# Optimization experiments

Measured on AMD Instinct MI355X. Metric: run time of the kernel, lower is better.

Reference implementation:

```python
import jax, jax.numpy as jnp
import numpy as np

RANGE_DISP = 32
IND_INPUT_VIEW = np.array([1, 9]) - 1  # 0-based indices of the two input views
TOTAL_VIEWS = 9                         # an_sparse + an_novel
FEAT_CH = 64


def conv2d(x, w, b):
    # x: (N, Cin, H, W), w: (Cout, Cin, kh, kw), SAME padding, stride 1
    y = jax.lax.conv_general_dilated(x, w, (1, 1), 'SAME',
                                     dimension_numbers=('NCHW', 'OIHW', 'NCHW'))
    return y + b[None, :, None, None]


def unfold_1xK(x, K):
    # torch.nn.functional.unfold(x, kernel_size=(1, K)) for x: (M, C, H, W)
    # -> (M, C, K, H*(W-K+1)), column index = h*(W-K+1) + w (row-major).
    M, C, H, W = x.shape
    out_w = W - K + 1
    cols = jnp.arange(out_w)[None, :] + jnp.arange(K)[:, None]  # (K, out_w)
    y = x[:, :, :, cols]             # (M, C, H, K, out_w)
    y = y.transpose(0, 1, 3, 2, 4)   # (M, C, K, H, out_w)
    return y.reshape(M, C, K, H * out_w)


def setup_inputs() -> dict:
    key = jax.random.key(0)
    ks = jax.random.split(key, 24)
    b, an_sparse, an_novel, rp = 2, 2, 7, 32
    K = RANGE_DISP
    ps = rp + K - 1  # 63

    def rn(k, shape, s=1.0):
        return jax.random.normal(k, shape, dtype=jnp.float32) * s

    W = 0.05  # weight init scale
    return {
        'lf_sparse':        rn(ks[0], (b, an_sparse, rp, ps)),
        'flow_sparse':      rn(ks[1], (b, an_sparse, rp, ps)),
        'warped_lf_sparse': rn(ks[2], (b, an_sparse, rp, ps)),
        'patch_left':       rn(ks[3], (b, an_novel, rp, rp)),
        'patch_right':      rn(ks[4], (b, an_novel, rp, rp)),
        # FlowRefNet: 3 -> 64 -> 64 -> 64, 3x3 convs, SAME
        'fr_w1': rn(ks[5], (FEAT_CH, 3, 3, 3), W), 'fr_b1': jnp.zeros((FEAT_CH,), jnp.float32),
        'fr_w2': rn(ks[6], (FEAT_CH, FEAT_CH, 3, 3), W), 'fr_b2': jnp.zeros((FEAT_CH,), jnp.float32),
        'fr_w3': rn(ks[7], (FEAT_CH, FEAT_CH, 3, 3), W), 'fr_b3': jnp.zeros((FEAT_CH,), jnp.float32),
        # MlpNet: per-disparity MLP 67 -> 64 -> 64 -> 1 (weight head) + conf head 64 -> 1
        'mlp_w1': rn(ks[8], (67, 64), W), 'mlp_b1': jnp.zeros((64,), jnp.float32),
        'mlp_w2': rn(ks[9], (64, 64), W), 'mlp_b2': jnp.zeros((64,), jnp.float32),
        'mlp_w3': rn(ks[10], (64, 1), W), 'mlp_b3': jnp.zeros((1,), jnp.float32),
        'conf_w': rn(ks[11], (64, 1), W), 'conf_b': jnp.zeros((1,), jnp.float32),
        # ViewRefNet: 3 -> 64 -> 64 -> 1 convs, residual on novel patch
        'vr_w1': rn(ks[12], (FEAT_CH, 3, 3, 3), W), 'vr_b1': jnp.zeros((FEAT_CH,), jnp.float32),
        'vr_w2': rn(ks[13], (FEAT_CH, FEAT_CH, 3, 3), W), 'vr_b2': jnp.zeros((FEAT_CH,), jnp.float32),
        'vr_w3': rn(ks[14], (1, FEAT_CH, 3, 3), W), 'vr_b3': jnp.zeros((1,), jnp.float32),
    }


def reference(lf_sparse, flow_sparse, warped_lf_sparse, patch_left, patch_right,
              fr_w1, fr_b1, fr_w2, fr_b2, fr_w3, fr_b3,
              mlp_w1, mlp_b1, mlp_w2, mlp_b2, mlp_w3, mlp_b3, conf_w, conf_b,
              vr_w1, vr_b1, vr_w2, vr_b2, vr_w3, vr_b3):
    b, an_sparse, rp, ps = lf_sparse.shape
    an_novel = patch_left.shape[1]
    K = RANGE_DISP
    N = rp * rp

    lf = lf_sparse.reshape(b * an_sparse, 1, rp, ps)
    fl = flow_sparse.reshape(b * an_sparse, 1, rp, ps)
    wp = warped_lf_sparse.reshape(b * an_sparse, 1, rp, ps)

    # FlowRefNet: flow-feature extraction
    h = jax.nn.relu(conv2d(jnp.concatenate([fl, lf, wp], axis=1), fr_w1, fr_b1))
    h = jax.nn.relu(conv2d(h, fr_w2, fr_b2))
    feat = jax.nn.relu(conv2d(h, fr_w3, fr_b3))  # (b*as, 64, rp, ps)

    # angular code: input-view index minus novel-view index
    ind_novel = np.delete(np.arange(TOTAL_VIEWS), IND_INPUT_VIEW)
    ang = jnp.asarray(IND_INPUT_VIEW[None, :] - ind_novel[:, None], dtype=lf.dtype)  # (an, as)
    spatial = (jnp.arange(K) - K // 2).astype(lf.dtype)  # (K,)

    # EPI windows via unfold(kernel=(1, K))
    flow_unf = unfold_1xK(fl, K)[:, 0]  # (b*as, K, N)
    feat_unf = unfold_1xK(feat, K)      # (b*as, 64, K, N)

    sh = (b, an_novel, an_sparse)
    f_flow = jnp.broadcast_to(flow_unf.reshape(b, 1, an_sparse, 1, K, N),  sh + (1, K, N))
    f_feat = jnp.broadcast_to(feat_unf.reshape(b, 1, an_sparse, FEAT_CH, K, N), sh + (FEAT_CH, K, N))
    f_spat = jnp.broadcast_to(spatial.reshape(1, 1, 1, 1, K, 1),           sh + (1, K, N))
    f_ang  = jnp.broadcast_to(ang.reshape(1, an_novel, an_sparse, 1, 1, 1), sh + (1, K, N))
    features = jnp.concatenate([f_flow, f_feat, f_spat, f_ang], axis=3)  # (b, an, as, 67, K, N)
    # -> (b*an*as*N, K, 67) matching permute(0,3,2,1).reshape in torch
    features = features.transpose(0, 1, 2, 5, 4, 3).reshape(-1, K, 67)

    # MlpNet: per-disparity weight + per-sample confidence
    h1 = jax.nn.relu(features @ mlp_w1 + mlp_b1)
    h2 = jax.nn.relu(h1 @ mlp_w2 + mlp_b2)          # (M2, K, 64)
    weight = (h2 @ mlp_w3 + mlp_b3)[..., 0]         # (M2, K)
    conf = (h2.mean(axis=1) @ conf_w + conf_b)[..., 0]  # (M2,)

    weight = jax.nn.softmax(weight.reshape(b, an_novel, an_sparse, N, K), axis=-1)
    confs = jax.nn.softmax(conf.reshape(b, an_novel, an_sparse, N), axis=2)

    # disparity-weighted combination over EPI windows
    epi = unfold_1xK(lf, K)[:, 0].reshape(b, an_sparse, K, N)
    nv = jnp.einsum('bskn,bvsnk->bvsn', epi, weight)   # (b, an, as, N)
    novel = (nv * confs).sum(axis=2)                   # (b, an, N)

    # ViewRefNet: residual refinement
    pn = novel.reshape(b * an_novel, 1, rp, rp)
    pl = patch_left.reshape(b * an_novel, 1, rp, rp)
    pr = patch_right.reshape(b * an_novel, 1, rp, rp)
    g = jax.nn.relu(conv2d(jnp.concatenate([pn, pl, pr], axis=1), vr_w1, vr_b1))
    g = jax.nn.relu(conv2d(g, vr_w2, vr_b2))
    res = conv2d(g, vr_w3, vr_b3)
    out = pn + res
    return out.reshape(b, an_novel, rp, rp)
```

## Files before the change

kernel.cpp:

```cpp
#include <hip/hip_runtime.h>

typedef unsigned short u16;
typedef unsigned int u32;
typedef __bf16 bf16x8 __attribute__((ext_vector_type(8)));
typedef float f32x4 __attribute__((ext_vector_type(4)));
typedef u16 u16x8 __attribute__((ext_vector_type(8)));

__device__ __forceinline__ u16 f2bf(float f) {
    __bf16 h = (__bf16)f;
    return __builtin_bit_cast(u16, h);
}
__device__ __forceinline__ float bf2f(u16 u) {
    unsigned int x = ((unsigned int)u) << 16;
    return __builtin_bit_cast(float, x);
}

union FragU { u16x8 u; bf16x8 v; };

constexpr size_t WB2F  = 0;
constexpr size_t WB3F  = 18432;
constexpr size_t WBV2  = 36864;
constexpr size_t W1T   = 55296;
constexpr size_t W2T   = 57344;
constexpr size_t X1    = 59392;
constexpr size_t X2    = 317440;
constexpr size_t FEATBF= 575488;
constexpr size_t NVOFF = 833536;
constexpr size_t CFOFF = 862208;
constexpr size_t NOVEL = 890880;
constexpr size_t Y1    = 905216;
constexpr size_t Y2    = 1363968;

__global__ __launch_bounds__(256) void conv1feat_kernel(
    const float* __restrict__ in0, const float* __restrict__ in1,
    const float* __restrict__ in2,
    const float* __restrict__ wts, const float* __restrict__ bias,
    u16* __restrict__ out,
    const float* __restrict__ frw2, const float* __restrict__ frw3,
    const float* __restrict__ vrw2,
    const float* __restrict__ mw1, const float* __restrict__ mw2,
    u16* __restrict__ wb2, u16* __restrict__ wb3, u16* __restrict__ wbv,
    u16* __restrict__ w1t, u16* __restrict__ w2t)
{
    constexpr int W = 63, NPX = 2016, H = 32;
    const int t = threadIdx.x;
    if (blockIdx.z == 4) {
        const int tid = (blockIdx.y * 8 + blockIdx.x) * 256 + t;
        for (int i = tid; i < 36864; i += 16384) {
            int tap = i >> 12, och = (i >> 6) & 63, cin = i & 63;
            size_t s = (size_t)och * 576 + cin * 9 + tap;
            wb2[i] = f2bf(frw2[s]);
            wb3[i] = f2bf(frw3[s]);
            wbv[i] = f2bf(vrw2[s]);
        }
        for (int i = tid; i < 4096; i += 16384) {
            int col = i >> 6, r = i & 63;
            w1t[i] = f2bf(mw1[(1 + r) * 64 + col]);
            w2t[i] = f2bf(mw2[r * 64 + col]);
        }
        return;
    }
    const int px = blockIdx.y * 256 + t;
    const int m = blockIdx.z;
    const int og = blockIdx.x;
    if (px >= NPX) return;
    const int y = px / W, x = px - y * W;

    float acc[8];
#pragma unroll
    for (int oc = 0; oc < 8; ++oc) acc[oc] = bias[og * 8 + oc];

#pragma unroll
    for (int cin = 0; cin < 3; ++cin) {
        const float* ip = (cin == 0 ? in0 : (cin == 1 ? in1 : in2)) + (size_t)m * NPX;
        float tap[9];
#pragma unroll
        for (int dy = 0; dy < 3; ++dy) {
            int yy = y + dy - 1;
            bool ry = (yy >= 0) && (yy < H);
#pragma unroll
            for (int dx = 0; dx < 3; ++dx) {
                int xx = x + dx - 1;
                tap[dy * 3 + dx] = (ry && xx >= 0 && xx < W) ? ip[yy * W + xx] : 0.f;
            }
        }
#pragma unroll
        for (int oc = 0; oc < 8; ++oc) {
            const float* wr = wts + (size_t)(og * 8 + oc) * 27 + cin * 9;
#pragma unroll
            for (int j = 0; j < 9; ++j) acc[oc] = fmaf(tap[j], wr[j], acc[oc]);
        }
    }
    u16x8 pk;
#pragma unroll
    for (int oc = 0; oc < 8; ++oc) pk[oc] = f2bf(fmaxf(acc[oc], 0.f));
    *(u16x8*)(out + ((size_t)m * NPX + px) * 64 + og * 8) = pk;
}

template<int W, int NPX>
__global__ __launch_bounds__(256) void convmfma_kernel(
    const u16* __restrict__ in, const u16* __restrict__ wbf,
    const float* __restrict__ bias, u16* __restrict__ out)
{
    constexpr int H = 32;
    const int t = threadIdx.x;
    const int base = blockIdx.x * 64;
    const int m = blockIdx.y;
    const int w = t >> 6, lane = t & 63, q = lane >> 4, l15 = lane & 15;

    const u16* im = in + (size_t)m * NPX * 64;
    const int pxA = base + w * 16 + l15;
    const int yA = pxA / W, xA = pxA - yA * W;
    const bool pxok = (pxA < NPX);

    f32x4 acc[4];
#pragma unroll
    for (int nt = 0; nt < 4; ++nt) acc[nt] = f32x4{0.f, 0.f, 0.f, 0.f};

#pragma unroll
    for (int tap = 0; tap < 9; ++tap) {
        const int dy = tap / 3 - 1, dx = tap % 3 - 1;
        const bool valid = pxok && (yA + dy >= 0) && (yA + dy < H)
                                && (xA + dx >= 0) && (xA + dx < W);
        const u16* ap = im + (size_t)(pxA + dy * W + dx) * 64;
        FragU a0, a1;
        if (valid) {
            a0 = *(const FragU*)(ap + q * 8);
            a1 = *(const FragU*)(ap + 32 + q * 8);
        } else {
#pragma unroll
            for (int jj = 0; jj < 8; ++jj) { a0.u[jj] = 0; a1.u[jj] = 0; }
        }
#pragma unroll
        for (int nt = 0; nt < 4; ++nt) {
            const u16* bp = wbf + tap * 4096 + (nt * 16 + l15) * 64;
            FragU b0 = *(const FragU*)(bp + q * 8);
            FragU b1 = *(const FragU*)(bp + 32 + q * 8);
            acc[nt] = __builtin_amdgcn_mfma_f32_16x16x32_bf16(a0.v, b0.v, acc[nt], 0, 0, 0);
            acc[nt] = __builtin_amdgcn_mfma_f32_16x16x32_bf16(a1.v, b1.v, acc[nt], 0, 0, 0);
        }
    }

#pragma unroll
    for (int nt = 0; nt < 4; ++nt) {
        const float bb = bias[nt * 16 + l15];
#pragma unroll
        for (int e = 0; e < 4; ++e) {
            int pxs = base + w * 16 + q * 4 + e;
            if (pxs < NPX)
                out[((size_t)m * NPX + pxs) * 64 + nt * 16 + l15] =
                    f2bf(fmaxf(acc[nt][e] + bb, 0.f));
        }
    }
}

__global__ __launch_bounds__(256, 2) void mlp_mfma_kernel(
    const float* __restrict__ lf, const float* __restrict__ flow,
    const u16* __restrict__ feat,
    const u16* __restrict__ w1t, const u16* __restrict__ w2t,
    const float* __restrict__ w1, const float* __restrict__ b1,
    const float* __restrict__ b2,
    const float* __restrict__ w3, const float* __restrict__ b3g,
    const float* __restrict__ cw, const float* __restrict__ cbg,
    float* __restrict__ nv_out, float* __restrict__ cf_out)
{
    constexpr int SBS = 72;
    __shared__ __align__(16) float s_vec[7 * 64];
    __shared__ __align__(16) float s_flow[256];
    __shared__ __align__(16) float s_epi[256];
    __shared__ __align__(16) u16 s_base[256 * SBS];

    const int t = threadIdx.x;
    const int blk = blockIdx.x;
    const int v = blk >> 9;
    const int r9_ = blk & 511;
    const int bs = r9_ >> 7;
    const int n0 = (r9_ & 127) * 8;
    const int b = bs >> 1, s = bs & 1;
    const int w = t >> 6, lane = t & 63, q = lane >> 4, l15 = lane & 15;

    if (t < 64) {
        s_vec[t]       = b1[t];
        s_vec[64 + t]  = b2[t];
        s_vec[128 + t] = w3[t];
        s_vec[192 + t] = cw[t];
        s_vec[256 + t] = w1[t];
        s_vec[320 + t] = w1[65 * 64 + t];
        s_vec[384 + t] = w1[66 * 64 + t];
    }
    {
        int nl = t >> 5, k = t & 31;
        int n = n0 + nl;
        int a = (bs * 32 + (n >> 5)) * 63 + (n & 31) + k;
        s_flow[t] = flow[a];
        s_epi[t]  = lf[a];
    }
    __syncthreads();

    const float b3s = b3g[0];
    const float cbs = cbg[0];

    FragU w1b[2][4];
#pragma unroll
    for (int ks = 0; ks < 2; ++ks)
#pragma unroll
        for (int nt = 0; nt < 4; ++nt)
            w1b[ks][nt] = *(const FragU*)(w1t + (nt * 16 + l15) * 64 + ks * 32 + q * 8);

    float w1r0pl[4], w1r65pl[4], b1pl[4];
#pragma unroll
    for (int nt = 0; nt < 4; ++nt) {
        int j1 = nt * 16 + l15;
        w1r0pl[nt]  = s_vec[256 + j1];
        w1r65pl[nt] = s_vec[320 + j1];
        b1pl[nt]    = s_vec[j1];
    }

#pragma unroll
    for (int mt = 0; mt < 4; ++mt) {
        const int rbase = w * 64 + mt * 16;
        FragU af[2];
        {
            int r = rbase + l15;
            int n = n0 + (r >> 5);
            int pos = (n >> 5) * 63 + (n & 31) + (r & 31);
            const u16* fp = feat + ((size_t)bs * 2016 + pos) * 64;
            af[0] = *(const FragU*)(fp + q * 8);
            af[1] = *(const FragU*)(fp + 32 + q * 8);
        }
        f32x4 flow4 = *(const f32x4*)(s_flow + rbase + q * 4);
#pragma unroll
        for (int nt = 0; nt < 4; ++nt) {
            f32x4 d = {0.f, 0.f, 0.f, 0.f};
            d = __builtin_amdgcn_mfma_f32_16x16x32_bf16(af[0].v, w1b[0][nt].v, d, 0, 0, 0);
            d = __builtin_amdgcn_mfma_f32_16x16x32_bf16(af[1].v, w1b[1][nt].v, d, 0, 0, 0);
#pragma unroll
            for (int e = 0; e < 4; ++e) {
                int r = rbase + q * 4 + e;
                int k = r & 31;
                float val = d[e] + flow4[e] * w1r0pl[nt]
                          + (float)(k - 16) * w1r65pl[nt] + b1pl[nt];
                s_base[r * SBS + nt * 16 + l15] = f2bf(val);
            }
        }
    }
    __syncthreads();

    FragU w2a[4][2];
#pragma unroll
    for (int mt = 0; mt < 4; ++mt)
#pragma unroll
        for (int ks = 0; ks < 2; ++ks)
            w2a[mt][ks] = *(const FragU*)(w2t + (mt * 16 + l15) * 64 + ks * 32 + q * 8);

    float w66pl[2][8];
#pragma unroll
    for (int ks = 0; ks < 2; ++ks)
#pragma unroll
        for (int jj = 0; jj < 8; ++jj)
            w66pl[ks][jj] = s_vec[384 + ks * 32 + q * 8 + jj];

    float b2pl[4][4], w3pl[4][4], cwpl[4][4];
#pragma unroll
    for (int mt = 0; mt < 4; ++mt)
#pragma unroll
        for (int e = 0; e < 4; ++e) {
            b2pl[mt][e] = s_vec[64 + mt * 16 + q * 4 + e];
            w3pl[mt][e] = s_vec[128 + mt * 16 + q * 4 + e];
            cwpl[mt][e] = s_vec[192 + mt * 16 + q * 4 + e];
        }
    float epi_pl[4];
#pragma unroll
    for (int nt = 0; nt < 4; ++nt) epi_pl[nt] = s_epi[w * 64 + nt * 16 + l15];

    const float ang = (s == 0) ? -(float)(v + 1) : (float)(7 - v);
    f32x4 acc[4][4];
#pragma unroll
    for (int nt = 0; nt < 4; ++nt) {
        FragU bfr[2];
#pragma unroll
        for (int ks = 0; ks < 2; ++ks) {
            const u16x8 raw = *(const u16x8*)(s_base + (w * 64 + nt * 16 + l15) * SBS + ks * 32 + q * 8);
#pragma unroll
            for (int jj = 0; jj < 8; ++jj) {
                float xv = bf2f(raw[jj]);
                float hv = fmaxf(xv + ang * w66pl[ks][jj], 0.f);
                bfr[ks].u[jj] = f2bf(hv);
            }
        }
#pragma unroll
        for (int mt = 0; mt < 4; ++mt) {
            f32x4 d = {0.f, 0.f, 0.f, 0.f};
            d = __builtin_amdgcn_mfma_f32_16x16x32_bf16(w2a[mt][0].v, bfr[0].v, d, 0, 0, 0);
            d = __builtin_amdgcn_mfma_f32_16x16x32_bf16(w2a[mt][1].v, bfr[1].v, d, 0, 0, 0);
            acc[mt][nt] = d;
        }
    }
    float wl[4], cfl[4];
#pragma unroll
    for (int nt = 0; nt < 4; ++nt) {
        float wls = 0.f, cfs = 0.f;
#pragma unroll
        for (int mt = 0; mt < 4; ++mt)
#pragma unroll
            for (int e = 0; e < 4; ++e) {
                float h2 = fmaxf(acc[mt][nt][e] + b2pl[mt][e], 0.f);
                wls += h2 * w3pl[mt][e];
                cfs += h2 * cwpl[mt][e];
            }
        wls += __shfl_xor(wls, 16); wls += __shfl_xor(wls, 32);
        cfs += __shfl_xor(cfs, 16); cfs += __shfl_xor(cfs, 32);
        wl[nt]  = wls + b3s;
        cfl[nt] = cfs;
    }
#pragma unroll
    for (int ni = 0; ni < 2; ++ni) {
        float a0 = wl[ni * 2], a1 = wl[ni * 2 + 1];
        float mx = fmaxf(a0, a1);
#pragma unroll
        for (int msk = 1; msk <= 8; msk <<= 1) mx = fmaxf(mx, __shfl_xor(mx, msk));
        float e0 = __expf(a0 - mx), e1 = __expf(a1 - mx);
        float ssum = e0 + e1;
        float nvp = e0 * epi_pl[ni * 2] + e1 * epi_pl[ni * 2 + 1];
        float cfp = cfl[ni * 2] + cfl[ni * 2 + 1];
#pragma unroll
        for (int msk = 1; msk <= 8; msk <<= 1) {
            ssum += __shfl_xor(ssum, msk);
            nvp  += __shfl_xor(nvp, msk);
            cfp  += __shfl_xor(cfp, msk);
        }
        if (lane == 0) {
            int n = n0 + w * 2 + ni;
            size_t idx = ((size_t)(b * 7 + v) * 2 + s) * 1024 + n;
            nv_out[idx] = nvp / ssum;
            cf_out[idx] = cfp * (1.f / 32.f) + cbs;
        }
    }
}

__global__ __launch_bounds__(256) void refconv1_kernel(
    const float* __restrict__ nv, const float* __restrict__ cf,
    const float* __restrict__ pl, const float* __restrict__ pr,
    const float* __restrict__ wts, const float* __restrict__ bias,
    u16* __restrict__ out, float* __restrict__ novel)
{
    __shared__ float pn[10][32];
    const int t = threadIdx.x;
    const int og = blockIdx.x, pt = blockIdx.y, m = blockIdx.z;
    const int y0 = pt * 8;

    for (int i = t; i < 320; i += 256) {
        int ri = i >> 5, col = i & 31;
        int gy = y0 - 1 + ri;
        float vv = 0.f;
        if (gy >= 0 && gy < 32) {
            int n = gy * 32 + col;
            size_t i0 = ((size_t)m * 2) * 1024 + n;
            size_t i1 = i0 + 1024;
            float c0 = cf[i0], c1 = cf[i1];
            float mx = fmaxf(c0, c1);
            float e0 = __expf(c0 - mx), e1 = __expf(c1 - mx);
            vv = (e0 * nv[i0] + e1 * nv[i1]) / (e0 + e1);
        }
        pn[ri][col] = vv;
    }
    __syncthreads();

    const int px = y0 * 32 + t;
    const int y = px >> 5, x = px & 31;
    if (og == 0) novel[(size_t)m * 1024 + px] = pn[y - y0 + 1][x];

    float acc[8];
#pragma unroll
    for (int oc = 0; oc < 8; ++oc) acc[oc] = bias[og * 8 + oc];

    {
        float tap[9];
#pragma unroll
        for (int dy = 0; dy < 3; ++dy) {
#pragma unroll
            for (int dx = 0; dx < 3; ++dx) {
                int gx = x + dx - 1;
                tap[dy * 3 + dx] = (gx >= 0 && gx < 32) ? pn[y - y0 + dy][gx] : 0.f;
            }
        }
#pragma unroll
        for (int oc = 0; oc < 8; ++oc) {
            const float* wr = wts + (size_t)(og * 8 + oc) * 27;
#pragma unroll
            for (int j = 0; j < 9; ++j) acc[oc] = fmaf(tap[j], wr[j], acc[oc]);
        }
    }
#pragma unroll
    for (int cin = 1; cin < 3; ++cin) {
        const float* ip = (cin == 1 ? pl : pr) + (size_t)m * 1024;
        float tap[9];
#pragma unroll
        for (int dy = 0; dy < 3; ++dy) {
            int yy = y + dy - 1;
            bool ry = (yy >= 0) && (yy < 32);
#pragma unroll
            for (int dx = 0; dx < 3; ++dx) {
                int xx = x + dx - 1;
                tap[dy * 3 + dx] = (ry && xx >= 0 && xx < 32) ? ip[yy * 32 + xx] : 0.f;
            }
        }
#pragma unroll
        for (int oc = 0; oc < 8; ++oc) {
            const float* wr = wts + (size_t)(og * 8 + oc) * 27 + cin * 9;
#pragma unroll
            for (int j = 0; j < 9; ++j) acc[oc] = fmaf(tap[j], wr[j], acc[oc]);
        }
    }
    u16x8 pk;
#pragma unroll
    for (int oc = 0; oc < 8; ++oc) pk[oc] = f2bf(fmaxf(acc[oc], 0.f));
    *(u16x8*)(out + ((size_t)m * 1024 + px) * 64 + og * 8) = pk;
}

__global__ __launch_bounds__(256) void convlast_kernel(
    const u16* __restrict__ in,
    const float* __restrict__ wts,
    const float* __restrict__ bias,
    const float* __restrict__ resid,
    float* __restrict__ out)
{
    __shared__ float sw3[576];
    const int t = threadIdx.x;
    for (int i = t; i < 576; i += 256) sw3[i] = wts[i];
    __syncthreads();

    const int tid = blockIdx.x * 256 + t;
    const int m = tid >> 10, p = tid & 1023;
    const int y = p >> 5, x = p & 31;
    float a = bias[0] + resid[tid];
    const u16* im = in + ((size_t)m * 1024 + p) * 64;
#pragma unroll
    for (int dy = 0; dy < 3; ++dy) {
        int yy = y + dy - 1;
        if (yy < 0 || yy >= 32) continue;
#pragma unroll
        for (int dx = 0; dx < 3; ++dx) {
            int xx = x + dx - 1;
            if (xx < 0 || xx >= 32) continue;
            const u16* ip = im + (size_t)((dy - 1) * 32 + (dx - 1)) * 64;
            const int tap = dy * 3 + dx;
#pragma unroll
            for (int cg = 0; cg < 8; ++cg) {
                u16x8 raw = *(const u16x8*)(ip + cg * 8);
#pragma unroll
                for (int e = 0; e < 8; ++e)
                    a = fmaf(bf2f(raw[e]), sw3[(cg * 8 + e) * 9 + tap], a);
            }
        }
    }
    out[tid] = a;
}

extern "C" void kernel_launch(void* const* d_in, const int* in_sizes, int n_in,
                              void* d_out, int out_size, void* d_ws, size_t ws_size,
                              hipStream_t stream) {
    const float* lf   = (const float*)d_in[0];
    const float* flow = (const float*)d_in[1];
    const float* wp   = (const float*)d_in[2];
    const float* pl   = (const float*)d_in[3];
    const float* pr   = (const float*)d_in[4];
    float* ws = (float*)d_ws;

    conv1feat_kernel<<<dim3(8, 8, 5), 256, 0, stream>>>(
        flow, lf, wp, (const float*)d_in[5], (const float*)d_in[6],
        (u16*)(ws + X1),
        (const float*)d_in[7], (const float*)d_in[9], (const float*)d_in[21],
        (const float*)d_in[11], (const float*)d_in[13],
        (u16*)(ws + WB2F), (u16*)(ws + WB3F), (u16*)(ws + WBV2),
        (u16*)(ws + W1T), (u16*)(ws + W2T));

    convmfma_kernel<63, 2016><<<dim3(32, 4), 256, 0, stream>>>(
        (const u16*)(ws + X1), (const u16*)(ws + WB2F), (const float*)d_in[8],
        (u16*)(ws + X2));
    convmfma_kernel<63, 2016><<<dim3(32, 4), 256, 0, stream>>>(
        (const u16*)(ws + X2), (const u16*)(ws + WB3F), (const float*)d_in[10],
        (u16*)(ws + FEATBF));

    mlp_mfma_kernel<<<3584, 256, 0, stream>>>(
        lf, flow, (const u16*)(ws + FEATBF),
        (const u16*)(ws + W1T), (const u16*)(ws + W2T),
        (const float*)d_in[11], (const float*)d_in[12],
        (const float*)d_in[14],
        (const float*)d_in[15], (const float*)d_in[16],
        (const float*)d_in[17], (const float*)d_in[18],
        ws + NVOFF, ws + CFOFF);

    refconv1_kernel<<<dim3(8, 4, 14), 256, 0, stream>>>(
        ws + NVOFF, ws + CFOFF, pl, pr,
        (const float*)d_in[19], (const float*)d_in[20],
        (u16*)(ws + Y1), ws + NOVEL);
    convmfma_kernel<32, 1024><<<dim3(16, 14), 256, 0, stream>>>(
        (const u16*)(ws + Y1), (const u16*)(ws + WBV2), (const float*)d_in[22],
        (u16*)(ws + Y2));
    convlast_kernel<<<56, 256, 0, stream>>>(
        (const u16*)(ws + Y2), (const float*)d_in[23], (const float*)d_in[24],
        ws + NOVEL, (float*)d_out);
}
```

Before: 216.8 us.

## Hoist view-independent MLP first layer into separate kernel and split conv output channels

The first MLP layer (features @ w1 plus the flow and disparity terms) does not depend on the novel view. It was recomputed in each of the 7 view blocks and is now computed once into a global bf16 buffer by a new 512-block kernel. The per-view kernel then reads that buffer instead of shared memory, with the view-dependent w1 row-66 term still applied per view. Separately, the MFMA conv kernels split the 64 output channels across two blocks to double the grid size, at the cost of loading the input activations twice. The trade is an extra launch and a large global round-trip for the intermediate in exchange for removing redundant matrix work.

After: 203.7 us. -6.0%, faster.

```diff
diff --git a/kernel.cpp b/kernel.cpp
--- a/kernel.cpp
+++ b/kernel.cpp
@@ -25,11 +25,12 @@
 constexpr size_t X1    = 59392;
 constexpr size_t X2    = 317440;
 constexpr size_t FEATBF= 575488;
-constexpr size_t NVOFF = 833536;
-constexpr size_t CFOFF = 862208;
-constexpr size_t NOVEL = 890880;
-constexpr size_t Y1    = 905216;
-constexpr size_t Y2    = 1363968;
+constexpr size_t BASEG = 833536;
+constexpr size_t NVOFF = 5027840;
+constexpr size_t CFOFF = 5056512;
+constexpr size_t NOVEL = 5085184;
+constexpr size_t Y1    = 5099520;
+constexpr size_t Y2    = 5558272;
 
 __global__ __launch_bounds__(256) void conv1feat_kernel(
     const float* __restrict__ in0, const float* __restrict__ in1,
@@ -105,7 +106,8 @@
     constexpr int H = 32;
     const int t = threadIdx.x;
     const int base = blockIdx.x * 64;
-    const int m = blockIdx.y;
+    const int ochb = blockIdx.y * 32;
+    const int m = blockIdx.z;
     const int w = t >> 6, lane = t & 63, q = lane >> 4, l15 = lane & 15;
 
     const u16* im = in + (size_t)m * NPX * 64;
@@ -113,9 +115,9 @@
     const int yA = pxA / W, xA = pxA - yA * W;
     const bool pxok = (pxA < NPX);
 
-    f32x4 acc[4];
-#pragma unroll
-    for (int nt = 0; nt < 4; ++nt) acc[nt] = f32x4{0.f, 0.f, 0.f, 0.f};
+    f32x4 acc[2];
+#pragma unroll
+    for (int nt = 0; nt < 2; ++nt) acc[nt] = f32x4{0.f, 0.f, 0.f, 0.f};
 
 #pragma unroll
     for (int tap = 0; tap < 9; ++tap) {
@@ -132,8 +134,8 @@
             for (int jj = 0; jj < 8; ++jj) { a0.u[jj] = 0; a1.u[jj] = 0; }
         }
 #pragma unroll
-        for (int nt = 0; nt < 4; ++nt) {
-            const u16* bp = wbf + tap * 4096 + (nt * 16 + l15) * 64;
+        for (int nt = 0; nt < 2; ++nt) {
+            const u16* bp = wbf + tap * 4096 + (ochb + nt * 16 + l15) * 64;
             FragU b0 = *(const FragU*)(bp + q * 8);
             FragU b1 = *(const FragU*)(bp + 32 + q * 8);
             acc[nt] = __builtin_amdgcn_mfma_f32_16x16x32_bf16(a0.v, b0.v, acc[nt], 0, 0, 0);
@@ -142,63 +144,46 @@
     }
 
 #pragma unroll
-    for (int nt = 0; nt < 4; ++nt) {
-        const float bb = bias[nt * 16 + l15];
+    for (int nt = 0; nt < 2; ++nt) {
+        const float bb = bias[ochb + nt * 16 + l15];
 #pragma unroll
         for (int e = 0; e < 4; ++e) {
             int pxs = base + w * 16 + q * 4 + e;
             if (pxs < NPX)
-                out[((size_t)m * NPX + pxs) * 64 + nt * 16 + l15] =
+                out[((size_t)m * NPX + pxs) * 64 + ochb + nt * 16 + l15] =
                     f2bf(fmaxf(acc[nt][e] + bb, 0.f));
         }
     }
 }
 
-__global__ __launch_bounds__(256, 2) void mlp_mfma_kernel(
-    const float* __restrict__ lf, const float* __restrict__ flow,
+__global__ __launch_bounds__(256, 2) void mlp_base_kernel(
+    const float* __restrict__ flow,
     const u16* __restrict__ feat,
-    const u16* __restrict__ w1t, const u16* __restrict__ w2t,
+    const u16* __restrict__ w1t,
     const float* __restrict__ w1, const float* __restrict__ b1,
-    const float* __restrict__ b2,
-    const float* __restrict__ w3, const float* __restrict__ b3g,
-    const float* __restrict__ cw, const float* __restrict__ cbg,
-    float* __restrict__ nv_out, float* __restrict__ cf_out)
+    u16* __restrict__ baseg)
 {
-    constexpr int SBS = 72;
-    __shared__ __align__(16) float s_vec[7 * 64];
+    __shared__ __align__(16) float s_vec[3 * 64];
     __shared__ __align__(16) float s_flow[256];
-    __shared__ __align__(16) float s_epi[256];
-    __shared__ __align__(16) u16 s_base[256 * SBS];
 
     const int t = threadIdx.x;
     const int blk = blockIdx.x;
-    const int v = blk >> 9;
-    const int r9_ = blk & 511;
-    const int bs = r9_ >> 7;
-    const int n0 = (r9_ & 127) * 8;
-    const int b = bs >> 1, s = bs & 1;
+    const int bs = blk >> 7;
+    const int n0 = (blk & 127) * 8;
     const int w = t >> 6, lane = t & 63, q = lane >> 4, l15 = lane & 15;
 
     if (t < 64) {
         s_vec[t]       = b1[t];
-        s_vec[64 + t]  = b2[t];
-        s_vec[128 + t] = w3[t];
-        s_vec[192 + t] = cw[t];
-        s_vec[256 + t] = w1[t];
-        s_vec[320 + t] = w1[65 * 64 + t];
-        s_vec[384 + t] = w1[66 * 64 + t];
+        s_vec[64 + t]  = w1[t];
+        s_vec[128 + t] = w1[65 * 64 + t];
     }
     {
         int nl = t >> 5, k = t & 31;
         int n = n0 + nl;
         int a = (bs * 32 + (n >> 5)) * 63 + (n & 31) + k;
         s_flow[t] = flow[a];
-        s_epi[t]  = lf[a];
     }
     __syncthreads();
-
-    const float b3s = b3g[0];
-    const float cbs = cbg[0];
 
     FragU w1b[2][4];
 #pragma unroll
@@ -211,9 +196,9 @@
 #pragma unroll
     for (int nt = 0; nt < 4; ++nt) {
         int j1 = nt * 16 + l15;
-        w1r0pl[nt]  = s_vec[256 + j1];
-        w1r65pl[nt] = s_vec[320 + j1];
         b1pl[nt]    = s_vec[j1];
+        w1r0pl[nt]  = s_vec[64 + j1];
+        w1r65pl[nt] = s_vec[128 + j1];
     }
 
 #pragma unroll
@@ -238,13 +223,52 @@
             for (int e = 0; e < 4; ++e) {
                 int r = rbase + q * 4 + e;
                 int k = r & 31;
+                int n = n0 + (r >> 5);
                 float val = d[e] + flow4[e] * w1r0pl[nt]
                           + (float)(k - 16) * w1r65pl[nt] + b1pl[nt];
-                s_base[r * SBS + nt * 16 + l15] = f2bf(val);
-            }
-        }
+                baseg[(((size_t)bs * 1024 + n) * 32 + k) * 64 + nt * 16 + l15] = f2bf(val);
+            }
+        }
+    }
+}
+
+__global__ __launch_bounds__(256, 2) void mlp_views_kernel(
+    const float* __restrict__ lf,
+    const u16* __restrict__ baseg,
+    const u16* __restrict__ w2t,
+    const float* __restrict__ w1, const float* __restrict__ b2,
+    const float* __restrict__ w3, const float* __restrict__ b3g,
+    const float* __restrict__ cw, const float* __restrict__ cbg,
+    float* __restrict__ nv_out, float* __restrict__ cf_out)
+{
+    __shared__ __align__(16) float s_vec[4 * 64];
+    __shared__ __align__(16) float s_epi[256];
+
+    const int t = threadIdx.x;
+    const int blk = blockIdx.x;
+    const int v = blk >> 9;
+    const int r9_ = blk & 511;
+    const int bs = r9_ >> 7;
+    const int n0 = (r9_ & 127) * 8;
+    const int b = bs >> 1, s = bs & 1;
+    const int w = t >> 6, lane = t & 63, q = lane >> 4, l15 = lane & 15;
+
+    if (t < 64) {
+        s_vec[t]       = b2[t];
+        s_vec[64 + t]  = w3[t];
+        s_vec[128 + t] = cw[t];
+        s_vec[192 + t] = w1[66 * 64 + t];
+    }
+    {
+        int nl = t >> 5, k = t & 31;
+        int n = n0 + nl;
+        int a = (bs * 32 + (n >> 5)) * 63 + (n & 31) + k;
+        s_epi[t] = lf[a];
     }
     __syncthreads();
+
+    const float b3s = b3g[0];
+    const float cbs = cbg[0];
 
     FragU w2a[4][2];
 #pragma unroll
@@ -258,16 +282,16 @@
     for (int ks = 0; ks < 2; ++ks)
 #pragma unroll
         for (int jj = 0; jj < 8; ++jj)
-            w66pl[ks][jj] = s_vec[384 + ks * 32 + q * 8 + jj];
+            w66pl[ks][jj] = s_vec[192 + ks * 32 + q * 8 + jj];
 
     float b2pl[4][4], w3pl[4][4], cwpl[4][4];
 #pragma unroll
     for (int mt = 0; mt < 4; ++mt)
 #pragma unroll
         for (int e = 0; e < 4; ++e) {
-            b2pl[mt][e] = s_vec[64 + mt * 16 + q * 4 + e];
-            w3pl[mt][e] = s_vec[128 + mt * 16 + q * 4 + e];
-            cwpl[mt][e] = s_vec[192 + mt * 16 + q * 4 + e];
+            b2pl[mt][e] = s_vec[mt * 16 + q * 4 + e];
+            w3pl[mt][e] = s_vec[64 + mt * 16 + q * 4 + e];
+            cwpl[mt][e] = s_vec[128 + mt * 16 + q * 4 + e];
         }
     float epi_pl[4];
 #pragma unroll
@@ -277,10 +301,13 @@
     f32x4 acc[4][4];
 #pragma unroll
     for (int nt = 0; nt < 4; ++nt) {
+        const int row = w * 64 + nt * 16 + l15;
+        const int n = n0 + (row >> 5), k = row & 31;
+        const u16* bp = baseg + (((size_t)bs * 1024 + n) * 32 + k) * 64;
         FragU bfr[2];
 #pragma unroll
         for (int ks = 0; ks < 2; ++ks) {
-            const u16x8 raw = *(const u16x8*)(s_base + (w * 64 + nt * 16 + l15) * SBS + ks * 32 + q * 8);
+            const u16x8 raw = *(const u16x8*)(bp + ks * 32 + q * 8);
 #pragma unroll
             for (int jj = 0; jj < 8; ++jj) {
                 float xv = bf2f(raw[jj]);
@@ -419,10 +446,8 @@
 }
 
 __global__ __launch_bounds__(256) void convlast_kernel(
-    const u16* __restrict__ in,
-    const float* __restrict__ wts,
-    const float* __restrict__ bias,
-    const float* __restrict__ resid,
+    const u16* __restrict__ in, const float* __restrict__ wts,
+    const float* __restrict__ bias, const float* __restrict__ resid,
     float* __restrict__ out)
 {
     __shared__ float sw3[576];
@@ -475,18 +500,21 @@
         (u16*)(ws + WB2F), (u16*)(ws + WB3F), (u16*)(ws + WBV2),
         (u16*)(ws + W1T), (u16*)(ws + W2T));
 
-    convmfma_kernel<63, 2016><<<dim3(32, 4), 256, 0, stream>>>(
+    convmfma_kernel<63, 2016><<<dim3(32, 2, 4), 256, 0, stream>>>(
         (const u16*)(ws + X1), (const u16*)(ws + WB2F), (const float*)d_in[8],
         (u16*)(ws + X2));
-    convmfma_kernel<63, 2016><<<dim3(32, 4), 256, 0, stream>>>(
+    convmfma_kernel<63, 2016><<<dim3(32, 2, 4), 256, 0, stream>>>(
         (const u16*)(ws + X2), (const u16*)(ws + WB3F), (const float*)d_in[10],
         (u16*)(ws + FEATBF));
 
-    mlp_mfma_kernel<<<3584, 256, 0, stream>>>(
-        lf, flow, (const u16*)(ws + FEATBF),
-        (const u16*)(ws + W1T), (const u16*)(ws + W2T),
+    mlp_base_kernel<<<512, 256, 0, stream>>>(
+        flow, (const u16*)(ws + FEATBF), (const u16*)(ws + W1T),
         (const float*)d_in[11], (const float*)d_in[12],
-        (const float*)d_in[14],
+        (u16*)(ws + BASEG));
+
+    mlp_views_kernel<<<3584, 256, 0, stream>>>(
+        lf, (const u16*)(ws + BASEG), (const u16*)(ws + W2T),
+        (const float*)d_in[11], (const float*)d_in[14],
         (const float*)d_in[15], (const float*)d_in[16],
         (const float*)d_in[17], (const float*)d_in[18],
         ws + NVOFF, ws + CFOFF);
@@ -495,7 +523,7 @@
         ws + NVOFF, ws + CFOFF, pl, pr,
         (const float*)d_in[19], (const float*)d_in[20],
         (u16*)(ws + Y1), ws + NOVEL);
-    convmfma_kernel<32, 1024><<<dim3(16, 14), 256, 0, stream>>>(
+    convmfma_kernel<32, 1024><<<dim3(16, 2, 14), 256, 0, stream>>>(
         (const u16*)(ws + Y1), (const u16*)(ws + WBV2), (const float*)d_in[22],
         (u16*)(ws + Y2));
     convlast_kernel<<<56, 256, 0, stream>>>(
```

## Split conv output channels across blocks and loop novel views inside MLP kernel

Applied to the files above, without the earlier changes.

The MFMA conv kernel now handles 32 output channels per block, with a new grid dimension over channel halves. This doubles block count for the small convs so more CUs are busy, at the cost of reloading the input fragments twice. The MLP kernel now loops over all 7 novel views inside one block instead of launching one block per view. The per-(b,s,n) setup, including feature staging into shared memory, is then shared across views, but the grid shrinks from 3584 to 512 blocks.

After: 186.7 us. 1.16x faster.

```diff
diff --git a/kernel.cpp b/kernel.cpp
--- a/kernel.cpp
+++ b/kernel.cpp
@@ -105,7 +105,8 @@
     constexpr int H = 32;
     const int t = threadIdx.x;
     const int base = blockIdx.x * 64;
-    const int m = blockIdx.y;
+    const int ochb = blockIdx.y * 32;
+    const int m = blockIdx.z;
     const int w = t >> 6, lane = t & 63, q = lane >> 4, l15 = lane & 15;
 
     const u16* im = in + (size_t)m * NPX * 64;
@@ -113,9 +114,9 @@
     const int yA = pxA / W, xA = pxA - yA * W;
     const bool pxok = (pxA < NPX);
 
-    f32x4 acc[4];
-#pragma unroll
-    for (int nt = 0; nt < 4; ++nt) acc[nt] = f32x4{0.f, 0.f, 0.f, 0.f};
+    f32x4 acc[2];
+#pragma unroll
+    for (int nt = 0; nt < 2; ++nt) acc[nt] = f32x4{0.f, 0.f, 0.f, 0.f};
 
 #pragma unroll
     for (int tap = 0; tap < 9; ++tap) {
@@ -132,8 +133,8 @@
             for (int jj = 0; jj < 8; ++jj) { a0.u[jj] = 0; a1.u[jj] = 0; }
         }
 #pragma unroll
-        for (int nt = 0; nt < 4; ++nt) {
-            const u16* bp = wbf + tap * 4096 + (nt * 16 + l15) * 64;
+        for (int nt = 0; nt < 2; ++nt) {
+            const u16* bp = wbf + tap * 4096 + (ochb + nt * 16 + l15) * 64;
             FragU b0 = *(const FragU*)(bp + q * 8);
             FragU b1 = *(const FragU*)(bp + 32 + q * 8);
             acc[nt] = __builtin_amdgcn_mfma_f32_16x16x32_bf16(a0.v, b0.v, acc[nt], 0, 0, 0);
@@ -142,13 +143,13 @@
     }
 
 #pragma unroll
-    for (int nt = 0; nt < 4; ++nt) {
-        const float bb = bias[nt * 16 + l15];
+    for (int nt = 0; nt < 2; ++nt) {
+        const float bb = bias[ochb + nt * 16 + l15];
 #pragma unroll
         for (int e = 0; e < 4; ++e) {
             int pxs = base + w * 16 + q * 4 + e;
             if (pxs < NPX)
-                out[((size_t)m * NPX + pxs) * 64 + nt * 16 + l15] =
+                out[((size_t)m * NPX + pxs) * 64 + ochb + nt * 16 + l15] =
                     f2bf(fmaxf(acc[nt][e] + bb, 0.f));
         }
     }
@@ -172,10 +173,8 @@
 
     const int t = threadIdx.x;
     const int blk = blockIdx.x;
-    const int v = blk >> 9;
-    const int r9_ = blk & 511;
-    const int bs = r9_ >> 7;
-    const int n0 = (r9_ & 127) * 8;
+    const int bs = blk >> 7;
+    const int n0 = (blk & 127) * 8;
     const int b = bs >> 1, s = bs & 1;
     const int w = t >> 6, lane = t & 63, q = lane >> 4, l15 = lane & 15;
 
@@ -273,67 +272,69 @@
 #pragma unroll
     for (int nt = 0; nt < 4; ++nt) epi_pl[nt] = s_epi[w * 64 + nt * 16 + l15];
 
-    const float ang = (s == 0) ? -(float)(v + 1) : (float)(7 - v);
-    f32x4 acc[4][4];
-#pragma unroll
-    for (int nt = 0; nt < 4; ++nt) {
-        FragU bfr[2];
-#pragma unroll
-        for (int ks = 0; ks < 2; ++ks) {
-            const u16x8 raw = *(const u16x8*)(s_base + (w * 64 + nt * 16 + l15) * SBS + ks * 32 + q * 8);
-#pragma unroll
-            for (int jj = 0; jj < 8; ++jj) {
-                float xv = bf2f(raw[jj]);
-                float hv = fmaxf(xv + ang * w66pl[ks][jj], 0.f);
-                bfr[ks].u[jj] = f2bf(hv);
-            }
-        }
-#pragma unroll
-        for (int mt = 0; mt < 4; ++mt) {
-            f32x4 d = {0.f, 0.f, 0.f, 0.f};
-            d = __builtin_amdgcn_mfma_f32_16x16x32_bf16(w2a[mt][0].v, bfr[0].v, d, 0, 0, 0);
-            d = __builtin_amdgcn_mfma_f32_16x16x32_bf16(w2a[mt][1].v, bfr[1].v, d, 0, 0, 0);
-            acc[mt][nt] = d;
-        }
-    }
-    float wl[4], cfl[4];
-#pragma unroll
-    for (int nt = 0; nt < 4; ++nt) {
-        float wls = 0.f, cfs = 0.f;
-#pragma unroll
-        for (int mt = 0; mt < 4; ++mt)
-#pragma unroll
-            for (int e = 0; e < 4; ++e) {
-                float h2 = fmaxf(acc[mt][nt][e] + b2pl[mt][e], 0.f);
-                wls += h2 * w3pl[mt][e];
-                cfs += h2 * cwpl[mt][e];
-            }
-        wls += __shfl_xor(wls, 16); wls += __shfl_xor(wls, 32);
-        cfs += __shfl_xor(cfs, 16); cfs += __shfl_xor(cfs, 32);
-        wl[nt]  = wls + b3s;
-        cfl[nt] = cfs;
-    }
-#pragma unroll
-    for (int ni = 0; ni < 2; ++ni) {
-        float a0 = wl[ni * 2], a1 = wl[ni * 2 + 1];
-        float mx = fmaxf(a0, a1);
-#pragma unroll
-        for (int msk = 1; msk <= 8; msk <<= 1) mx = fmaxf(mx, __shfl_xor(mx, msk));
-        float e0 = __expf(a0 - mx), e1 = __expf(a1 - mx);
-        float ssum = e0 + e1;
-        float nvp = e0 * epi_pl[ni * 2] + e1 * epi_pl[ni * 2 + 1];
-        float cfp = cfl[ni * 2] + cfl[ni * 2 + 1];
-#pragma unroll
-        for (int msk = 1; msk <= 8; msk <<= 1) {
-            ssum += __shfl_xor(ssum, msk);
-            nvp  += __shfl_xor(nvp, msk);
-            cfp  += __shfl_xor(cfp, msk);
-        }
-        if (lane == 0) {
-            int n = n0 + w * 2 + ni;
-            size_t idx = ((size_t)(b * 7 + v) * 2 + s) * 1024 + n;
-            nv_out[idx] = nvp / ssum;
-            cf_out[idx] = cfp * (1.f / 32.f) + cbs;
+    for (int v = 0; v < 7; ++v) {
+        float ang = (s == 0) ? -(float)(v + 1) : (float)(7 - v);
+        f32x4 acc[4][4];
+#pragma unroll
+        for (int nt = 0; nt < 4; ++nt) {
+            FragU bfr[2];
+#pragma unroll
+            for (int ks = 0; ks < 2; ++ks) {
+                const u16x8 raw = *(const u16x8*)(s_base + (w * 64 + nt * 16 + l15) * SBS + ks * 32 + q * 8);
+#pragma unroll
+                for (int jj = 0; jj < 8; ++jj) {
+                    float xv = bf2f(raw[jj]);
+                    float hv = fmaxf(xv + ang * w66pl[ks][jj], 0.f);
+                    bfr[ks].u[jj] = f2bf(hv);
+                }
+            }
+#pragma unroll
+            for (int mt = 0; mt < 4; ++mt) {
+                f32x4 d = {0.f, 0.f, 0.f, 0.f};
+                d = __builtin_amdgcn_mfma_f32_16x16x32_bf16(w2a[mt][0].v, bfr[0].v, d, 0, 0, 0);
+                d = __builtin_amdgcn_mfma_f32_16x16x32_bf16(w2a[mt][1].v, bfr[1].v, d, 0, 0, 0);
+                acc[mt][nt] = d;
+            }
+        }
+        float wl[4], cfl[4];
+#pragma unroll
+        for (int nt = 0; nt < 4; ++nt) {
+            float wls = 0.f, cfs = 0.f;
+#pragma unroll
+            for (int mt = 0; mt < 4; ++mt)
+#pragma unroll
+                for (int e = 0; e < 4; ++e) {
+                    float h2 = fmaxf(acc[mt][nt][e] + b2pl[mt][e], 0.f);
+                    wls += h2 * w3pl[mt][e];
+                    cfs += h2 * cwpl[mt][e];
+                }
+            wls += __shfl_xor(wls, 16); wls += __shfl_xor(wls, 32);
+            cfs += __shfl_xor(cfs, 16); cfs += __shfl_xor(cfs, 32);
+            wl[nt]  = wls + b3s;
+            cfl[nt] = cfs;
+        }
+#pragma unroll
+        for (int ni = 0; ni < 2; ++ni) {
+            float a0 = wl[ni * 2], a1 = wl[ni * 2 + 1];
+            float mx = fmaxf(a0, a1);
+#pragma unroll
+            for (int msk = 1; msk <= 8; msk <<= 1) mx = fmaxf(mx, __shfl_xor(mx, msk));
+            float e0 = __expf(a0 - mx), e1 = __expf(a1 - mx);
+            float ssum = e0 + e1;
+            float nvp = e0 * epi_pl[ni * 2] + e1 * epi_pl[ni * 2 + 1];
+            float cfp = cfl[ni * 2] + cfl[ni * 2 + 1];
+#pragma unroll
+            for (int msk = 1; msk <= 8; msk <<= 1) {
+                ssum += __shfl_xor(ssum, msk);
+                nvp  += __shfl_xor(nvp, msk);
+                cfp  += __shfl_xor(cfp, msk);
+            }
+            if (lane == 0) {
+                int n = n0 + w * 2 + ni;
+                size_t idx = ((size_t)(b * 7 + v) * 2 + s) * 1024 + n;
+                nv_out[idx] = nvp / ssum;
+                cf_out[idx] = cfp * (1.f / 32.f) + cbs;
+            }
         }
     }
 }
@@ -419,10 +420,8 @@
 }
 
 __global__ __launch_bounds__(256) void convlast_kernel(
-    const u16* __restrict__ in,
-    const float* __restrict__ wts,
-    const float* __restrict__ bias,
-    const float* __restrict__ resid,
+    const u16* __restrict__ in, const float* __restrict__ wts,
+    const float* __restrict__ bias, const float* __restrict__ resid,
     float* __restrict__ out)
 {
     __shared__ float sw3[576];
@@ -475,14 +474,14 @@
         (u16*)(ws + WB2F), (u16*)(ws + WB3F), (u16*)(ws + WBV2),
         (u16*)(ws + W1T), (u16*)(ws + W2T));
 
-    convmfma_kernel<63, 2016><<<dim3(32, 4), 256, 0, stream>>>(
+    convmfma_kernel<63, 2016><<<dim3(32, 2, 4), 256, 0, stream>>>(
         (const u16*)(ws + X1), (const u16*)(ws + WB2F), (const float*)d_in[8],
         (u16*)(ws + X2));
-    convmfma_kernel<63, 2016><<<dim3(32, 4), 256, 0, stream>>>(
+    convmfma_kernel<63, 2016><<<dim3(32, 2, 4), 256, 0, stream>>>(
         (const u16*)(ws + X2), (const u16*)(ws + WB3F), (const float*)d_in[10],
         (u16*)(ws + FEATBF));
 
-    mlp_mfma_kernel<<<3584, 256, 0, stream>>>(
+    mlp_mfma_kernel<<<512, 256, 0, stream>>>(
         lf, flow, (const u16*)(ws + FEATBF),
         (const u16*)(ws + W1T), (const u16*)(ws + W2T),
         (const float*)d_in[11], (const float*)d_in[12],
@@ -495,7 +494,7 @@
         ws + NVOFF, ws + CFOFF, pl, pr,
         (const float*)d_in[19], (const float*)d_in[20],
         (u16*)(ws + Y1), ws + NOVEL);
-    convmfma_kernel<32, 1024><<<dim3(16, 14), 256, 0, stream>>>(
+    convmfma_kernel<32, 1024><<<dim3(16, 2, 14), 256, 0, stream>>>(
         (const u16*)(ws + Y1), (const u16*)(ws + WBV2), (const float*)d_in[22],
         (u16*)(ws + Y2));
     convlast_kernel<<<56, 256, 0, stream>>>(
```
